# Performance work log

Measured on AMD Instinct MI355X. Metric: run time of the kernel, lower is better.

Reference implementation:

```python
import jax, jax.numpy as jnp
import numpy as np

COLOR_SIZE = 4
SIZE = 128
LENGTH = SIZE * SIZE * 3  # 49152


def setup_inputs() -> dict:
    key = jax.random.key(0)
    k1, k2, k3, k4 = jax.random.split(key, 4)
    example = jax.random.randint(k1, (2, SIZE, SIZE, 3), 0, COLOR_SIZE, dtype=jnp.int32)
    W_in = jax.random.normal(k2, (1, 1024), dtype=jnp.float32) * 0.02
    pos_enc = jax.random.normal(k3, (LENGTH, 1024), dtype=jnp.float32)
    W_final = jax.random.normal(k4, (1024, COLOR_SIZE), dtype=jnp.float32) * 0.02
    b_final = jnp.zeros((COLOR_SIZE,), dtype=jnp.float32)
    return {"example": example, "W_in": W_in, "pos_enc": pos_enc,
            "W_final": W_final, "b_final": b_final}


def reference(example, W_in, pos_enc, W_final, b_final):
    # example: [B, 128, 128, 3] int, values in [0, color_size)
    B = example.shape[0]
    x = example.astype(jnp.float32) / COLOR_SIZE * 2.0 - 1.0
    x = x.reshape(B, LENGTH, 1)
    x = x * 2.0 - 1.0  # second scaling, as in original call()
    x = x @ W_in  # [B, L, 1] @ [1, F] -> [B, L, F]
    x = jax.nn.relu(x + pos_enc)
    # running-average via causal cumsum; factor computed in fp16 as in original
    factor = (1.0 / jnp.arange(1, LENGTH + 1, dtype=jnp.float32))
    factor = factor.astype(jnp.float16).astype(jnp.float32)[:, None]
    x = jnp.cumsum(x, axis=-2) * factor
    x = x @ W_final + b_final  # [B, L, color_size]
    x = x.reshape(B, SIZE, SIZE, 3, COLOR_SIZE)
    return x.astype(jnp.float32)
```

## Files before the change

### kernel.cpp

```cpp
#include <hip/hip_runtime.h>
#include <math.h>

#define L_TOTAL 49152
#define NBLK 512
#define ROWS_PER_BLK 96
#define ROWS_PER_WAVE 24

__device__ __forceinline__ float4 f4add(float4 a, float4 b) {
  return make_float4(a.x + b.x, a.y + b.y, a.z + b.z, a.w + b.w);
}

__device__ __forceinline__ float fp16_roundtrip_pos(float x) {
  unsigned u = __float_as_uint(x);
  int e = (int)((u >> 23) & 0xffu) - 127;
  unsigned m = (u & 0x7fffffu) | 0x800000u;
  int shift = (e >= -14) ? 13 : (13 + (-14 - e));
  if (shift >= 25) return 0.0f;
  unsigned keep = m >> shift;
  unsigned rem = m & ((1u << shift) - 1u);
  unsigned halfbit = 1u << (shift - 1);
  if (rem > halfbit || (rem == halfbit && (keep & 1u))) keep++;
  return ldexpf((float)keep, e + shift - 23);
}

__global__ __launch_bounds__(256, 2) void gpart_kernel(
    const int* __restrict__ ex, const float4* __restrict__ win4,
    const float4* __restrict__ pos4, const float4* __restrict__ wf4,
    float4* __restrict__ g4, float4* __restrict__ pp) {
  __shared__ float4 sg[2][ROWS_PER_BLK];
  __shared__ float4 wpart[2][4];

  const int lane = threadIdx.x & 63;
  const int wv = threadIdx.x >> 6;
  const int rowBase = blockIdx.x * ROWS_PER_BLK + wv * ROWS_PER_WAVE;

  float4 win[4];
  float4 wf[4][4];
#pragma unroll
  for (int j = 0; j < 4; ++j) {
    const int fi = j * 64 + lane;
    win[j] = win4[fi];
#pragma unroll
    for (int k = 0; k < 4; ++k) wf[j][k] = wf4[fi * 4 + k];
  }

  float4 bp0 = make_float4(0.f, 0.f, 0.f, 0.f);
  float4 bp1 = make_float4(0.f, 0.f, 0.f, 0.f);

  for (int r = 0; r < ROWS_PER_WAVE; ++r) {
    const int l = rowBase + r;
    const float s0 = (float)ex[l] - 3.0f;
    const float s1 = (float)ex[L_TOTAL + l] - 3.0f;
    float4 a0 = make_float4(0.f, 0.f, 0.f, 0.f);
    float4 a1 = make_float4(0.f, 0.f, 0.f, 0.f);
#pragma unroll
    for (int j = 0; j < 4; ++j) {
      const float4 p = pos4[(size_t)l * 256 + j * 64 + lane];
      const float pc[4] = {p.x, p.y, p.z, p.w};
      const float wc[4] = {win[j].x, win[j].y, win[j].z, win[j].w};
#pragma unroll
      for (int k = 0; k < 4; ++k) {
        const float t0 = fmaxf(fmaf(s0, wc[k], pc[k]), 0.0f);
        const float t1 = fmaxf(fmaf(s1, wc[k], pc[k]), 0.0f);
        const float4 w = wf[j][k];
        a0.x = fmaf(t0, w.x, a0.x); a0.y = fmaf(t0, w.y, a0.y);
        a0.z = fmaf(t0, w.z, a0.z); a0.w = fmaf(t0, w.w, a0.w);
        a1.x = fmaf(t1, w.x, a1.x); a1.y = fmaf(t1, w.y, a1.y);
        a1.z = fmaf(t1, w.z, a1.z); a1.w = fmaf(t1, w.w, a1.w);
      }
    }
#pragma unroll
    for (int off = 32; off > 0; off >>= 1) {
      a0.x += __shfl_xor(a0.x, off); a0.y += __shfl_xor(a0.y, off);
      a0.z += __shfl_xor(a0.z, off); a0.w += __shfl_xor(a0.w, off);
      a1.x += __shfl_xor(a1.x, off); a1.y += __shfl_xor(a1.y, off);
      a1.z += __shfl_xor(a1.z, off); a1.w += __shfl_xor(a1.w, off);
    }
    bp0 = f4add(bp0, a0);
    bp1 = f4add(bp1, a1);
    if (lane == 0) {
      sg[0][wv * ROWS_PER_WAVE + r] = a0;
      sg[1][wv * ROWS_PER_WAVE + r] = a1;
    }
  }

  if (lane == 0) { wpart[0][wv] = bp0; wpart[1][wv] = bp1; }
  __syncthreads();

  if (threadIdx.x < 2 * ROWS_PER_BLK) {
    const int bb = threadIdx.x / ROWS_PER_BLK;
    const int i = threadIdx.x - bb * ROWS_PER_BLK;
    g4[(size_t)bb * L_TOTAL + blockIdx.x * ROWS_PER_BLK + i] = sg[bb][i];
  }
  if (threadIdx.x < 2) {
    const int bb = threadIdx.x;
    pp[bb * NBLK + blockIdx.x] =
        f4add(f4add(wpart[bb][0], wpart[bb][1]),
              f4add(wpart[bb][2], wpart[bb][3]));
  }
}

__global__ __launch_bounds__(256, 2) void scan_kernel(
    const float4* __restrict__ g4, const float4* __restrict__ pp,
    const float* __restrict__ bfin, float4* __restrict__ out4) {
  __shared__ float4 sg[2][ROWS_PER_BLK];
  __shared__ float4 wq[2][4];
  __shared__ float4 boffs[2];

  const int tid = threadIdx.x;
  const int lane = tid & 63;
  const int wv = tid >> 6;
  const int bid = blockIdx.x;

  if (tid < 2 * ROWS_PER_BLK) {
    const int bb = tid / ROWS_PER_BLK;
    const int i = tid - bb * ROWS_PER_BLK;
    sg[bb][i] = g4[(size_t)bb * L_TOTAL + bid * ROWS_PER_BLK + i];
  }

  float4 q0 = make_float4(0.f, 0.f, 0.f, 0.f);
  float4 q1 = make_float4(0.f, 0.f, 0.f, 0.f);
  for (int jj = tid; jj < bid; jj += 256) {
    q0 = f4add(q0, pp[jj]);
    q1 = f4add(q1, pp[NBLK + jj]);
  }
#pragma unroll
  for (int off = 32; off > 0; off >>= 1) {
    q0.x += __shfl_xor(q0.x, off); q0.y += __shfl_xor(q0.y, off);
    q0.z += __shfl_xor(q0.z, off); q0.w += __shfl_xor(q0.w, off);
    q1.x += __shfl_xor(q1.x, off); q1.y += __shfl_xor(q1.y, off);
    q1.z += __shfl_xor(q1.z, off); q1.w += __shfl_xor(q1.w, off);
  }
  if (lane == 0) { wq[0][wv] = q0; wq[1][wv] = q1; }
  __syncthreads();
  if (tid == 0) {
    boffs[0] = f4add(f4add(wq[0][0], wq[0][1]), f4add(wq[0][2], wq[0][3]));
    boffs[1] = f4add(f4add(wq[1][0], wq[1][1]), f4add(wq[1][2], wq[1][3]));
  }
  __syncthreads();

  const bool act = tid < 2 * ROWS_PER_BLK;
  const int bb = tid / ROWS_PER_BLK;
  const int i = tid - bb * ROWS_PER_BLK;
#pragma unroll
  for (int d = 1; d < ROWS_PER_BLK; d <<= 1) {
    float4 addv = make_float4(0.f, 0.f, 0.f, 0.f);
    if (act && i >= d) addv = sg[bb][i - d];
    __syncthreads();
    if (act && i >= d) sg[bb][i] = f4add(sg[bb][i], addv);
    __syncthreads();
  }
  if (act) {
    const int l = bid * ROWS_PER_BLK + i;
    const float4 v = f4add(sg[bb][i], boffs[bb]);
    const float factor = fp16_roundtrip_pos(1.0f / (float)(l + 1));
    float4 o;
    o.x = fmaf(v.x, factor, bfin[0]);
    o.y = fmaf(v.y, factor, bfin[1]);
    o.z = fmaf(v.z, factor, bfin[2]);
    o.w = fmaf(v.w, factor, bfin[3]);
    out4[(size_t)bb * L_TOTAL + l] = o;
  }
}

extern "C" void kernel_launch(void* const* d_in, const int* in_sizes, int n_in,
                              void* d_out, int out_size, void* d_ws, size_t ws_size,
                              hipStream_t stream) {
  const int* ex = (const int*)d_in[0];
  const float4* win4 = (const float4*)d_in[1];
  const float4* pos4 = (const float4*)d_in[2];
  const float4* wf4 = (const float4*)d_in[3];
  const float* bfin = (const float*)d_in[4];
  float4* out4 = (float4*)d_out;

  float4* g4 = (float4*)d_ws;
  float4* pp = g4 + (size_t)2 * L_TOTAL;

  gpart_kernel<<<NBLK, 256, 0, stream>>>(ex, win4, pos4, wf4, g4, pp);
  scan_kernel<<<NBLK, 256, 0, stream>>>(g4, pp, bfin, out4);
}
```

Measured before the change: 48.01 us.

## Replace per-row shuffle reductions with LDS transpose reduce and in-wave scan

The per-row 64-lane butterfly reduction is replaced by staging four rows of partial sums in LDS and reducing them with a transposed read, followed by an in-wave prefix scan with a carry across batches. Per-wave totals are written, so the second kernel becomes a light finish pass with no LDS scan or block barriers. Block and wave row counts shrink and occupancy rises to three blocks per CU. This cuts cross-lane shuffle work in the pos_enc-bound main kernel, at the cost of more LDS traffic and a longer serial prefix over wave partials in the finish kernel.

```diff
diff --git a/kernel.cpp b/kernel.cpp
--- a/kernel.cpp
+++ b/kernel.cpp
@@ -2,9 +2,11 @@
 #include <math.h>
 
 #define L_TOTAL 49152
-#define NBLK 512
-#define ROWS_PER_BLK 96
-#define ROWS_PER_WAVE 24
+#define NBLK 768
+#define ROWS_PER_BLK 64
+#define ROWS_PER_WAVE 16
+#define NWGROUPS (NBLK * 4)
+#define SCR_STRIDE 520
 
 __device__ __forceinline__ float4 f4add(float4 a, float4 b) {
   return make_float4(a.x + b.x, a.y + b.y, a.z + b.z, a.w + b.w);
@@ -23,15 +25,15 @@
   return ldexpf((float)keep, e + shift - 23);
 }
 
-__global__ __launch_bounds__(256, 2) void gpart_kernel(
+__global__ __launch_bounds__(256, 3) void gpart_kernel(
     const int* __restrict__ ex, const float4* __restrict__ win4,
     const float4* __restrict__ pos4, const float4* __restrict__ wf4,
-    float4* __restrict__ g4, float4* __restrict__ pp) {
-  __shared__ float4 sg[2][ROWS_PER_BLK];
-  __shared__ float4 wpart[2][4];
+    float* __restrict__ gf, float* __restrict__ ppwf) {
+  __shared__ float scratch[4][4 * SCR_STRIDE];
 
   const int lane = threadIdx.x & 63;
   const int wv = threadIdx.x >> 6;
+  float* scr = scratch[wv];
   const int rowBase = blockIdx.x * ROWS_PER_BLK + wv * ROWS_PER_WAVE;
 
   float4 win[4];
@@ -44,123 +46,99 @@
     for (int k = 0; k < 4; ++k) wf[j][k] = wf4[fi * 4 + k];
   }
 
-  float4 bp0 = make_float4(0.f, 0.f, 0.f, 0.f);
-  float4 bp1 = make_float4(0.f, 0.f, 0.f, 0.f);
+  const int rhat = lane >> 4;
+  const int chat = (lane >> 1) & 7;
+  const int h = lane & 1;
 
-  for (int r = 0; r < ROWS_PER_WAVE; ++r) {
-    const int l = rowBase + r;
-    const float s0 = (float)ex[l] - 3.0f;
-    const float s1 = (float)ex[L_TOTAL + l] - 3.0f;
-    float4 a0 = make_float4(0.f, 0.f, 0.f, 0.f);
-    float4 a1 = make_float4(0.f, 0.f, 0.f, 0.f);
+  float carry = 0.0f;
+
+  for (int batch = 0; batch < 4; ++batch) {
 #pragma unroll
-    for (int j = 0; j < 4; ++j) {
-      const float4 p = pos4[(size_t)l * 256 + j * 64 + lane];
-      const float pc[4] = {p.x, p.y, p.z, p.w};
-      const float wc[4] = {win[j].x, win[j].y, win[j].z, win[j].w};
+    for (int r = 0; r < 4; ++r) {
+      const int l = rowBase + batch * 4 + r;
+      const float s0 = (float)ex[l] - 3.0f;
+      const float s1 = (float)ex[L_TOTAL + l] - 3.0f;
+      float4 a0 = make_float4(0.f, 0.f, 0.f, 0.f);
+      float4 a1 = make_float4(0.f, 0.f, 0.f, 0.f);
 #pragma unroll
-      for (int k = 0; k < 4; ++k) {
-        const float t0 = fmaxf(fmaf(s0, wc[k], pc[k]), 0.0f);
-        const float t1 = fmaxf(fmaf(s1, wc[k], pc[k]), 0.0f);
-        const float4 w = wf[j][k];
-        a0.x = fmaf(t0, w.x, a0.x); a0.y = fmaf(t0, w.y, a0.y);
-        a0.z = fmaf(t0, w.z, a0.z); a0.w = fmaf(t0, w.w, a0.w);
-        a1.x = fmaf(t1, w.x, a1.x); a1.y = fmaf(t1, w.y, a1.y);
-        a1.z = fmaf(t1, w.z, a1.z); a1.w = fmaf(t1, w.w, a1.w);
+      for (int j = 0; j < 4; ++j) {
+        const float4 p = pos4[(size_t)l * 256 + j * 64 + lane];
+        const float pc[4] = {p.x, p.y, p.z, p.w};
+        const float wc[4] = {win[j].x, win[j].y, win[j].z, win[j].w};
+#pragma unroll
+        for (int k = 0; k < 4; ++k) {
+          const float t0 = fmaxf(fmaf(s0, wc[k], pc[k]), 0.0f);
+          const float t1 = fmaxf(fmaf(s1, wc[k], pc[k]), 0.0f);
+          const float4 w = wf[j][k];
+          a0.x = fmaf(t0, w.x, a0.x); a0.y = fmaf(t0, w.y, a0.y);
+          a0.z = fmaf(t0, w.z, a0.z); a0.w = fmaf(t0, w.w, a0.w);
+          a1.x = fmaf(t1, w.x, a1.x); a1.y = fmaf(t1, w.y, a1.y);
+          a1.z = fmaf(t1, w.z, a1.z); a1.w = fmaf(t1, w.w, a1.w);
+        }
       }
+      float* dst = &scr[r * SCR_STRIDE + lane * 8];
+      *(float4*)(dst) = a0;
+      *(float4*)(dst + 4) = a1;
     }
+
+    const float* src = &scr[rhat * SCR_STRIDE + h * 32 * 8 + chat];
+    float s = 0.0f;
 #pragma unroll
-    for (int off = 32; off > 0; off >>= 1) {
-      a0.x += __shfl_xor(a0.x, off); a0.y += __shfl_xor(a0.y, off);
-      a0.z += __shfl_xor(a0.z, off); a0.w += __shfl_xor(a0.w, off);
-      a1.x += __shfl_xor(a1.x, off); a1.y += __shfl_xor(a1.y, off);
-      a1.z += __shfl_xor(a1.z, off); a1.w += __shfl_xor(a1.w, off);
+    for (int i = 0; i < 32; ++i) s += src[i * 8];
+    s += __shfl_xor(s, 1);
+
+    {
+      float u = __shfl_up(s, 16);
+      if (rhat >= 1) s += u;
+      u = __shfl_up(s, 32);
+      if (rhat >= 2) s += u;
     }
-    bp0 = f4add(bp0, a0);
-    bp1 = f4add(bp1, a1);
-    if (lane == 0) {
-      sg[0][wv * ROWS_PER_WAVE + r] = a0;
-      sg[1][wv * ROWS_PER_WAVE + r] = a1;
+    const float vout = s + carry;
+    carry = __shfl(vout, 48 + (lane & 15));
+
+    if (h == 0) {
+      const int row = rowBase + batch * 4 + rhat;
+      gf[(size_t)(chat >> 2) * L_TOTAL * 4 + (size_t)row * 4 + (chat & 3)] =
+          vout;
     }
   }
 
-  if (lane == 0) { wpart[0][wv] = bp0; wpart[1][wv] = bp1; }
-  __syncthreads();
-
-  if (threadIdx.x < 2 * ROWS_PER_BLK) {
-    const int bb = threadIdx.x / ROWS_PER_BLK;
-    const int i = threadIdx.x - bb * ROWS_PER_BLK;
-    g4[(size_t)bb * L_TOTAL + blockIdx.x * ROWS_PER_BLK + i] = sg[bb][i];
-  }
-  if (threadIdx.x < 2) {
-    const int bb = threadIdx.x;
-    pp[bb * NBLK + blockIdx.x] =
-        f4add(f4add(wpart[bb][0], wpart[bb][1]),
-              f4add(wpart[bb][2], wpart[bb][3]));
+  if (h == 0 && rhat == 0) {
+    const int wg = blockIdx.x * 4 + wv;
+    ppwf[(size_t)(chat >> 2) * NWGROUPS * 4 + (size_t)wg * 4 + (chat & 3)] =
+        carry;
   }
 }
 
-__global__ __launch_bounds__(256, 2) void scan_kernel(
-    const float4* __restrict__ g4, const float4* __restrict__ pp,
+__global__ __launch_bounds__(128, 8) void finish_kernel(
+    const float4* __restrict__ g4, const float4* __restrict__ ppw,
     const float* __restrict__ bfin, float4* __restrict__ out4) {
-  __shared__ float4 sg[2][ROWS_PER_BLK];
-  __shared__ float4 wq[2][4];
-  __shared__ float4 boffs[2];
+  const int tid = threadIdx.x;
+  const int bb = tid >> 6;
+  const int i = tid & 63;
+  const int bid = blockIdx.x;
+  const int wgBase = bid * 4;
 
-  const int tid = threadIdx.x;
-  const int lane = tid & 63;
-  const int wv = tid >> 6;
-  const int bid = blockIdx.x;
-
-  if (tid < 2 * ROWS_PER_BLK) {
-    const int bb = tid / ROWS_PER_BLK;
-    const int i = tid - bb * ROWS_PER_BLK;
-    sg[bb][i] = g4[(size_t)bb * L_TOTAL + bid * ROWS_PER_BLK + i];
-  }
-
-  float4 q0 = make_float4(0.f, 0.f, 0.f, 0.f);
-  float4 q1 = make_float4(0.f, 0.f, 0.f, 0.f);
-  for (int jj = tid; jj < bid; jj += 256) {
-    q0 = f4add(q0, pp[jj]);
-    q1 = f4add(q1, pp[NBLK + jj]);
-  }
+  float4 q = make_float4(0.f, 0.f, 0.f, 0.f);
+  for (int j = i; j < wgBase; j += 64) q = f4add(q, ppw[bb * NWGROUPS + j]);
 #pragma unroll
   for (int off = 32; off > 0; off >>= 1) {
-    q0.x += __shfl_xor(q0.x, off); q0.y += __shfl_xor(q0.y, off);
-    q0.z += __shfl_xor(q0.z, off); q0.w += __shfl_xor(q0.w, off);
-    q1.x += __shfl_xor(q1.x, off); q1.y += __shfl_xor(q1.y, off);
-    q1.z += __shfl_xor(q1.z, off); q1.w += __shfl_xor(q1.w, off);
+    q.x += __shfl_xor(q.x, off); q.y += __shfl_xor(q.y, off);
+    q.z += __shfl_xor(q.z, off); q.w += __shfl_xor(q.w, off);
   }
-  if (lane == 0) { wq[0][wv] = q0; wq[1][wv] = q1; }
-  __syncthreads();
-  if (tid == 0) {
-    boffs[0] = f4add(f4add(wq[0][0], wq[0][1]), f4add(wq[0][2], wq[0][3]));
-    boffs[1] = f4add(f4add(wq[1][0], wq[1][1]), f4add(wq[1][2], wq[1][3]));
-  }
-  __syncthreads();
+  const int gsub = i >> 4;
+  for (int k = 0; k < gsub; ++k)
+    q = f4add(q, ppw[bb * NWGROUPS + wgBase + k]);
 
-  const bool act = tid < 2 * ROWS_PER_BLK;
-  const int bb = tid / ROWS_PER_BLK;
-  const int i = tid - bb * ROWS_PER_BLK;
-#pragma unroll
-  for (int d = 1; d < ROWS_PER_BLK; d <<= 1) {
-    float4 addv = make_float4(0.f, 0.f, 0.f, 0.f);
-    if (act && i >= d) addv = sg[bb][i - d];
-    __syncthreads();
-    if (act && i >= d) sg[bb][i] = f4add(sg[bb][i], addv);
-    __syncthreads();
-  }
-  if (act) {
-    const int l = bid * ROWS_PER_BLK + i;
-    const float4 v = f4add(sg[bb][i], boffs[bb]);
-    const float factor = fp16_roundtrip_pos(1.0f / (float)(l + 1));
-    float4 o;
-    o.x = fmaf(v.x, factor, bfin[0]);
-    o.y = fmaf(v.y, factor, bfin[1]);
-    o.z = fmaf(v.z, factor, bfin[2]);
-    o.w = fmaf(v.w, factor, bfin[3]);
-    out4[(size_t)bb * L_TOTAL + l] = o;
-  }
+  const int row = bid * ROWS_PER_BLK + i;
+  const float4 v = f4add(g4[(size_t)bb * L_TOTAL + row], q);
+  const float factor = fp16_roundtrip_pos(1.0f / (float)(row + 1));
+  float4 o;
+  o.x = fmaf(v.x, factor, bfin[0]);
+  o.y = fmaf(v.y, factor, bfin[1]);
+  o.z = fmaf(v.z, factor, bfin[2]);
+  o.w = fmaf(v.w, factor, bfin[3]);
+  out4[(size_t)bb * L_TOTAL + row] = o;
 }
 
 extern "C" void kernel_launch(void* const* d_in, const int* in_sizes, int n_in,
@@ -173,9 +151,10 @@
   const float* bfin = (const float*)d_in[4];
   float4* out4 = (float4*)d_out;
 
-  float4* g4 = (float4*)d_ws;
-  float4* pp = g4 + (size_t)2 * L_TOTAL;
+  float* gf = (float*)d_ws;
+  float* ppwf = gf + (size_t)2 * L_TOTAL * 4;
 
-  gpart_kernel<<<NBLK, 256, 0, stream>>>(ex, win4, pos4, wf4, g4, pp);
-  scan_kernel<<<NBLK, 256, 0, stream>>>(g4, pp, bfin, out4);
+  gpart_kernel<<<NBLK, 256, 0, stream>>>(ex, win4, pos4, wf4, gf, ppwf);
+  finish_kernel<<<NBLK, 128, 0, stream>>>((const float4*)gf,
+                                          (const float4*)ppwf, bfin, out4);
 }
```

Result: slower. 54.85 us (+14.2%).
